# Optimization experiments

Measured on AMD Instinct MI355X. Metric: run time of the kernel, lower is better.

## Reference

```python
import jax, jax.numpy as jnp
import numpy as np

N_NODES = 100000
N_EDGES = 1600000
IN_FEATS = 128
OUT_FEATS = 128


def setup_inputs() -> dict:
    key = jax.random.key(0)
    k1, k2, k3, k4 = jax.random.split(key, 4)
    edge_data = jax.random.normal(k1, (N_EDGES, IN_FEATS), dtype=jnp.float32)
    dst = jax.random.randint(k2, (N_EDGES,), 0, N_NODES, dtype=jnp.int32)
    # nn.Linear(in_feats, out_feats) init scale ~ 1/sqrt(in_feats)
    s = 1.0 / np.sqrt(IN_FEATS)
    W = jax.random.uniform(k3, (OUT_FEATS, IN_FEATS), dtype=jnp.float32, minval=-s, maxval=s)
    b = jax.random.uniform(k4, (OUT_FEATS,), dtype=jnp.float32, minval=-s, maxval=s)
    return {"edge_data": edge_data, "dst": dst, "W": W, "b": b}


def reference(edge_data, dst, W, b):
    # Segment-mean of edge features into destination-node mailboxes.
    # DGL: h[v] = mean over incoming edges' 'h'; then ReLU(W h + b).
    sums = jax.ops.segment_sum(edge_data, dst, num_segments=N_NODES)  # [N, in]
    counts = jax.ops.segment_sum(jnp.ones((N_EDGES,), jnp.float32), dst,
                                 num_segments=N_NODES)  # [N]
    agg = sums / jnp.maximum(counts, 1.0)[:, None]  # mean; 0 for isolated nodes
    h = agg @ W.T + b  # [N, out]
    return jax.nn.relu(h)
```

## Files before the change

### kernel.cpp

```cpp
#include <hip/hip_runtime.h>

#define NEDGES 1600000
#define NNODES 100000
#define NF 128
#define NBUCK 391
#define NBLKA 391
#define NOFF  (NBUCK * NBLKA)
#define NSB   150

typedef short s16x8 __attribute__((ext_vector_type(8)));
typedef float f32x4 __attribute__((ext_vector_type(4)));

#define BH_B     0u
#define BHO_B    611584u
#define SST_B    1223168u
#define ROWPTR_B 1224448u
#define BKT_B    1624512u
#define EIDS_B   8024512u
#define WBF_B    14424512u

static __device__ __forceinline__ unsigned short f2bf(float x) {
    unsigned u = __float_as_uint(x);
    return (unsigned short)((u + 0x7fffu + ((u >> 16) & 1u)) >> 16);
}

__global__ __launch_bounds__(256) void k_bhist(const int* __restrict__ dst,
                                               int* __restrict__ bh,
                                               const float* __restrict__ W,
                                               unsigned short* __restrict__ Wb) {
    __shared__ int cnt[NBUCK];
    const int t = threadIdx.x, b = blockIdx.x;
    const int g = b * 256 + t;
    if (g < NF * NF) Wb[g] = f2bf(W[g]);
    for (int k = t; k < NBUCK; k += 256) cnt[k] = 0;
    __syncthreads();
    const int base = b * 4096;
    #pragma unroll
    for (int j = 0; j < 4; ++j) {
        const int i = base + j * 1024 + t * 4;
        if (i + 4 <= NEDGES) {
            const int4 d = *(const int4*)(dst + i);
            atomicAdd(&cnt[d.x >> 8], 1);
            atomicAdd(&cnt[d.y >> 8], 1);
            atomicAdd(&cnt[d.z >> 8], 1);
            atomicAdd(&cnt[d.w >> 8], 1);
        } else {
            for (int e = i; e < NEDGES; ++e) atomicAdd(&cnt[dst[e] >> 8], 1);
        }
    }
    __syncthreads();
    for (int k = t; k < NBUCK; k += 256) bh[k * NBLKA + b] = cnt[k];
}

__global__ __launch_bounds__(256) void k_scanB(const int* __restrict__ in,
                                               int* __restrict__ outp,
                                               unsigned long long* __restrict__ state) {
    const int t = threadIdx.x, b = blockIdx.x;
    const int lane = t & 63, wv = t >> 6;
    const int i0 = b * 1024 + t * 4;
    int v0 = 0, v1 = 0, v2 = 0, v3 = 0;
    if (i0 + 4 <= NOFF) {
        const int4 q = *(const int4*)(in + i0);
        v0 = q.x; v1 = q.y; v2 = q.z; v3 = q.w;
    } else if (i0 < NOFF) {
        v0 = in[i0];
        if (i0 + 1 < NOFF) v1 = in[i0 + 1];
        if (i0 + 2 < NOFF) v2 = in[i0 + 2];
    }
    const int tsum = v0 + v1 + v2 + v3;
    int winc = tsum;
    #pragma unroll
    for (int d = 1; d < 64; d <<= 1) {
        const int u = __shfl_up(winc, d, 64);
        if (lane >= d) winc += u;
    }
    __shared__ int wsum[4];
    __shared__ int xbase;
    if (lane == 63) wsum[wv] = winc;
    __syncthreads();
    int woff = 0;
    #pragma unroll
    for (int w = 0; w < 3; ++w)
        if (wv > w) woff += wsum[w];
    const int tot = wsum[0] + wsum[1] + wsum[2] + wsum[3];

    if (wv == 0) {
        if (b > 0) {
            if (lane == 0)
                __hip_atomic_store(&state[b],
                                   ((unsigned long long)1 << 32) | (unsigned)tot,
                                   __ATOMIC_RELEASE, __HIP_MEMORY_SCOPE_AGENT);
            int excl = 0;
            int p = b - 1;
            for (;;) {
                const int idx = p - lane;
                unsigned long long s;
                do {
                    s = (idx >= 0)
                        ? __hip_atomic_load(&state[idx], __ATOMIC_ACQUIRE,
                                            __HIP_MEMORY_SCOPE_AGENT)
                        : ((unsigned long long)2 << 32);
                    if (!(s >> 32)) __builtin_amdgcn_s_sleep(2);
                } while (__any(!(s >> 32)));
                const unsigned long long m2 = __ballot((s >> 32) == 2);
                const int f = m2 ? (__ffsll((long long)m2) - 1) : 63;
                int c = (lane <= f) ? (int)(unsigned)s : 0;
                #pragma unroll
                for (int d = 32; d > 0; d >>= 1) c += __shfl_xor(c, d, 64);
                excl += c;
                if (m2) break;
                p -= 64;
            }
            if (lane == 0) {
                __hip_atomic_store(&state[b],
                                   ((unsigned long long)2 << 32) |
                                       (unsigned)(excl + tot),
                                   __ATOMIC_RELEASE, __HIP_MEMORY_SCOPE_AGENT);
                xbase = excl;
            }
        } else {
            if (lane == 0) {
                __hip_atomic_store(&state[0],
                                   ((unsigned long long)2 << 32) | (unsigned)tot,
                                   __ATOMIC_RELEASE, __HIP_MEMORY_SCOPE_AGENT);
                xbase = 0;
            }
        }
    }
    __syncthreads();

    const int base = xbase + woff + (winc - tsum);
    if (i0 + 4 <= NOFF) {
        int4 r;
        r.x = base; r.y = base + v0; r.z = base + v0 + v1; r.w = base + v0 + v1 + v2;
        *(int4*)(outp + i0) = r;
    } else if (i0 < NOFF) {
        outp[i0] = base;
        if (i0 + 1 < NOFF) outp[i0 + 1] = base + v0;
        if (i0 + 2 < NOFF) outp[i0 + 2] = base + v0 + v1;
    }
}

__global__ __launch_bounds__(256) void k_scatterA(const int* __restrict__ dst,
                                                  const int* __restrict__ bhoff,
                                                  unsigned* __restrict__ bucketed) {
    __shared__ int cur[NBUCK];
    const int t = threadIdx.x, b = blockIdx.x;
    for (int k = t; k < NBUCK; k += 256) cur[k] = 0;
    __syncthreads();
    const int base = b * 4096;
    #pragma unroll
    for (int j = 0; j < 4; ++j) {
        const int i = base + j * 1024 + t * 4;
        if (i + 4 <= NEDGES) {
            const int4 d = *(const int4*)(dst + i);
            const int r0 = atomicAdd(&cur[d.x >> 8], 1);
            const int r1 = atomicAdd(&cur[d.y >> 8], 1);
            const int r2 = atomicAdd(&cur[d.z >> 8], 1);
            const int r3 = atomicAdd(&cur[d.w >> 8], 1);
            bucketed[bhoff[(d.x >> 8) * NBLKA + b] + r0] =
                ((unsigned)(i + 0) << 8) | (unsigned)(d.x & 255);
            bucketed[bhoff[(d.y >> 8) * NBLKA + b] + r1] =
                ((unsigned)(i + 1) << 8) | (unsigned)(d.y & 255);
            bucketed[bhoff[(d.z >> 8) * NBLKA + b] + r2] =
                ((unsigned)(i + 2) << 8) | (unsigned)(d.z & 255);
            bucketed[bhoff[(d.w >> 8) * NBLKA + b] + r3] =
                ((unsigned)(i + 3) << 8) | (unsigned)(d.w & 255);
        } else {
            for (int e = i; e < NEDGES; ++e) {
                const int d = dst[e];
                const int r = atomicAdd(&cur[d >> 8], 1);
                bucketed[bhoff[(d >> 8) * NBLKA + b] + r] =
                    ((unsigned)e << 8) | (unsigned)(d & 255);
            }
        }
    }
}

__global__ __launch_bounds__(256) void k_bucket(const unsigned* __restrict__ bucketed,
                                                const int* __restrict__ bhoff,
                                                int* __restrict__ rowptr,
                                                unsigned* __restrict__ eids) {
    __shared__ int cnt[256], rnk[256], exc[256];
    __shared__ int wtot[4];
    const int t = threadIdx.x, k = blockIdx.x;
    const int lane = t & 63, wv = t >> 6;
    cnt[t] = 0;
    rnk[t] = 0;
    __syncthreads();
    const int ebase = bhoff[k * NBLKA];
    const int eend  = (k + 1 < NBUCK) ? bhoff[(k + 1) * NBLKA] : NEDGES;
    const int ecnt  = eend - ebase;

    for (int i = t; i < ecnt; i += 256)
        atomicAdd(&cnt[bucketed[ebase + i] & 255u], 1);
    __syncthreads();

    const int own = cnt[t];
    int incl = own;
    #pragma unroll
    for (int d = 1; d < 64; d <<= 1) {
        const int u = __shfl_up(incl, d, 64);
        if (lane >= d) incl += u;
    }
    if (lane == 63) wtot[wv] = incl;
    __syncthreads();
    int woff = 0;
    #pragma unroll
    for (int w = 0; w < 3; ++w)
        if (wv > w) woff += wtot[w];
    exc[t] = woff + incl - own;
    __syncthreads();

    const int node = k * 256 + t;
    if (node < NNODES) rowptr[node] = ebase + exc[t];
    if (k == 0 && t == 0) rowptr[NNODES] = NEDGES;

    for (int i = t; i < ecnt; i += 256) {
        const unsigned u = bucketed[ebase + i];
        const int local = (int)(u & 255u);
        const int r = atomicAdd(&rnk[local], 1);
        eids[ebase + exc[local] + r] = ((u >> 8) << 4) | (unsigned)(local & 15);
    }
}

__global__ __launch_bounds__(256) void k_fused(
        const float* __restrict__ edge, const int* __restrict__ rowptr,
        const unsigned* __restrict__ eids, const unsigned short* __restrict__ Wb,
        const float* __restrict__ bias, float* __restrict__ out) {
    __shared__ float aggf[16][132];
    __shared__ __align__(16) char aggb[16 * 256];
    const int tid  = threadIdx.x;
    const int lane = tid & 63;
    const int wv   = tid >> 6;
    const int l15  = lane & 15;
    const int l4   = lane >> 4;
    const int n0   = blockIdx.x * 16;

    for (int idx = tid; idx < 16 * 132; idx += 256)
        (&aggf[0][0])[idx] = 0.0f;
    __syncthreads();

    const int eb    = rowptr[n0];
    const int ee    = rowptr[n0 + 16];
    const int chunk = (ee - eb + 3) >> 2;
    const int wcs   = eb + wv * chunk;
    const int wce   = min(wcs + chunk, ee);

    int   cur = -1;
    float a0 = 0.f, a1 = 0.f;

    for (int base = wcs; base < wce; base += 64) {
        const int m = min(64, wce - base);
        const unsigned ev = (lane < m) ? eids[base + lane] : 0u;
        int b = 0;
        for (; b + 16 <= m; b += 16) {
            unsigned id[16];
            int      rw[16];
            #pragma unroll
            for (int j = 0; j < 16; ++j) {
                const unsigned u = (unsigned)__builtin_amdgcn_readlane((int)ev, b + j);
                id[j] = u >> 4;
                rw[j] = (int)(u & 15u);
            }
            float2 xv[16];
            #pragma unroll
            for (int j = 0; j < 16; ++j)
                xv[j] = *(const float2*)(edge + (size_t)id[j] * NF + lane * 2);
            #pragma unroll
            for (int j = 0; j < 16; ++j) {
                if (rw[j] != cur) {
                    if (cur >= 0) {
                        atomicAdd(&aggf[cur][lane], a0);
                        atomicAdd(&aggf[cur][64 + lane], a1);
                    }
                    cur = rw[j];
                    a0 = 0.f; a1 = 0.f;
                }
                a0 += xv[j].x;
                a1 += xv[j].y;
            }
        }
        for (; b < m; ++b) {
            const unsigned u = (unsigned)__builtin_amdgcn_readlane((int)ev, b);
            const float2 v = *(const float2*)(edge + (size_t)(u >> 4) * NF + lane * 2);
            const int r = (int)(u & 15u);
            if (r != cur) {
                if (cur >= 0) {
                    atomicAdd(&aggf[cur][lane], a0);
                    atomicAdd(&aggf[cur][64 + lane], a1);
                }
                cur = r;
                a0 = 0.f; a1 = 0.f;
            }
            a0 += v.x;
            a1 += v.y;
        }
    }
    if (cur >= 0) {
        atomicAdd(&aggf[cur][lane], a0);
        atomicAdd(&aggf[cur][64 + lane], a1);
    }
    __syncthreads();

    {
        const int r  = tid >> 4;
        const int p0 = (tid & 15) * 4;
        const int cs = rowptr[n0 + r];
        const int ce = rowptr[n0 + r + 1];
        const float inv = 1.0f / fmaxf((float)(ce - cs), 1.0f);
        const float4 xv = *(const float4*)&aggf[r][p0];
        const float4 yv = *(const float4*)&aggf[r][64 + p0];
        const float xa[4] = {xv.x, xv.y, xv.z, xv.w};
        const float ya[4] = {yv.x, yv.y, yv.z, yv.w};
        #pragma unroll
        for (int j = 0; j < 4; ++j) {
            const unsigned pk = (unsigned)f2bf(xa[j] * inv) |
                                ((unsigned)f2bf(ya[j] * inv) << 16);
            const int byt = ((r * 256 + (p0 + j) * 4) ^ ((r & 7) << 4));
            *(unsigned*)(aggb + byt) = pk;
        }
    }
    __syncthreads();

    #pragma unroll
    for (int t = 0; t < 2; ++t) {
        const int j0 = (wv * 2 + t) * 16;
        f32x4 acc = {0.f, 0.f, 0.f, 0.f};
        #pragma unroll
        for (int ks = 0; ks < 4; ++ks) {
            const s16x8 wfv = *(const s16x8*)((const char*)Wb +
                                              (j0 + l15) * 256 + ks * 64 + l4 * 16);
            const int byt = ((l15 * 256 + ks * 64 + l4 * 16) ^ ((l15 & 7) << 4));
            const s16x8 av = *(const s16x8*)(aggb + byt);
            acc = __builtin_amdgcn_mfma_f32_16x16x32_bf16(av, wfv, acc, 0, 0, 0);
        }
        const float bj = bias[j0 + l15];
        #pragma unroll
        for (int r = 0; r < 4; ++r) {
            const int m = l4 * 4 + r;
            out[(size_t)(n0 + m) * NF + j0 + l15] = fmaxf(acc[r] + bj, 0.f);
        }
    }
}

extern "C" void kernel_launch(void* const* d_in, const int* in_sizes, int n_in,
                              void* d_out, int out_size, void* d_ws, size_t ws_size,
                              hipStream_t stream) {
    const float* edge = (const float*)d_in[0];
    const int*   dst  = (const int*)d_in[1];
    const float* W    = (const float*)d_in[2];
    const float* b    = (const float*)d_in[3];
    float* out = (float*)d_out;

    char* ws = (char*)d_ws;
    int*                bh       = (int*)(ws + BH_B);
    int*                bhoff    = (int*)(ws + BHO_B);
    unsigned long long* sstate   = (unsigned long long*)(ws + SST_B);
    int*                rowptr   = (int*)(ws + ROWPTR_B);
    unsigned*           bucketed = (unsigned*)(ws + BKT_B);
    unsigned*           eids     = (unsigned*)(ws + EIDS_B);
    unsigned short*     Wb       = (unsigned short*)(ws + WBF_B);

    hipMemsetAsync(ws + SST_B, 0, 1280, stream);

    k_bhist<<<NBLKA, 256, 0, stream>>>(dst, bh, W, Wb);
    k_scanB<<<NSB, 256, 0, stream>>>(bh, bhoff, sstate);
    k_scatterA<<<NBLKA, 256, 0, stream>>>(dst, bhoff, bucketed);
    k_bucket<<<NBUCK, 256, 0, stream>>>(bucketed, bhoff, rowptr, eids);
    k_fused<<<NNODES / 16, 256, 0, stream>>>(edge, rowptr, eids, Wb, b, out);
}
```

Before: 240.2 us.

## Fold scan-state memset into histogram kernel, use nontemporal accesses, coalesce output stores

```diff
diff --git a/kernel.cpp b/kernel.cpp
--- a/kernel.cpp
+++ b/kernel.cpp
@@ -27,11 +27,13 @@
 __global__ __launch_bounds__(256) void k_bhist(const int* __restrict__ dst,
                                                int* __restrict__ bh,
                                                const float* __restrict__ W,
-                                               unsigned short* __restrict__ Wb) {
+                                               unsigned short* __restrict__ Wb,
+                                               unsigned long long* __restrict__ sstate) {
     __shared__ int cnt[NBUCK];
     const int t = threadIdx.x, b = blockIdx.x;
     const int g = b * 256 + t;
     if (g < NF * NF) Wb[g] = f2bf(W[g]);
+    if (b == 0 && t < 160) sstate[t] = 0ull;
     for (int k = t; k < NBUCK; k += 256) cnt[k] = 0;
     __syncthreads();
     const int base = b * 4096;
@@ -158,14 +160,14 @@
             const int r1 = atomicAdd(&cur[d.y >> 8], 1);
             const int r2 = atomicAdd(&cur[d.z >> 8], 1);
             const int r3 = atomicAdd(&cur[d.w >> 8], 1);
-            bucketed[bhoff[(d.x >> 8) * NBLKA + b] + r0] =
-                ((unsigned)(i + 0) << 8) | (unsigned)(d.x & 255);
-            bucketed[bhoff[(d.y >> 8) * NBLKA + b] + r1] =
-                ((unsigned)(i + 1) << 8) | (unsigned)(d.y & 255);
-            bucketed[bhoff[(d.z >> 8) * NBLKA + b] + r2] =
-                ((unsigned)(i + 2) << 8) | (unsigned)(d.z & 255);
-            bucketed[bhoff[(d.w >> 8) * NBLKA + b] + r3] =
-                ((unsigned)(i + 3) << 8) | (unsigned)(d.w & 255);
+            __builtin_nontemporal_store(((unsigned)(i + 0) << 8) | (unsigned)(d.x & 255),
+                                        bucketed + bhoff[(d.x >> 8) * NBLKA + b] + r0);
+            __builtin_nontemporal_store(((unsigned)(i + 1) << 8) | (unsigned)(d.y & 255),
+                                        bucketed + bhoff[(d.y >> 8) * NBLKA + b] + r1);
+            __builtin_nontemporal_store(((unsigned)(i + 2) << 8) | (unsigned)(d.z & 255),
+                                        bucketed + bhoff[(d.z >> 8) * NBLKA + b] + r2);
+            __builtin_nontemporal_store(((unsigned)(i + 3) << 8) | (unsigned)(d.w & 255),
+                                        bucketed + bhoff[(d.w >> 8) * NBLKA + b] + r3);
         } else {
             for (int e = i; e < NEDGES; ++e) {
                 const int d = dst[e];
@@ -220,7 +222,8 @@
         const unsigned u = bucketed[ebase + i];
         const int local = (int)(u & 255u);
         const int r = atomicAdd(&rnk[local], 1);
-        eids[ebase + exc[local] + r] = ((u >> 8) << 4) | (unsigned)(local & 15);
+        __builtin_nontemporal_store(((u >> 8) << 4) | (unsigned)(local & 15),
+                                    eids + ebase + exc[local] + r);
     }
 }
 
@@ -265,8 +268,11 @@
             }
             float2 xv[16];
             #pragma unroll
-            for (int j = 0; j < 16; ++j)
-                xv[j] = *(const float2*)(edge + (size_t)id[j] * NF + lane * 2);
+            for (int j = 0; j < 16; ++j) {
+                const double dv = __builtin_nontemporal_load(
+                    (const double*)(edge + (size_t)id[j] * NF + lane * 2));
+                __builtin_memcpy(&xv[j], &dv, 8);
+            }
             #pragma unroll
             for (int j = 0; j < 16; ++j) {
                 if (rw[j] != cur) {
@@ -339,8 +345,19 @@
         #pragma unroll
         for (int r = 0; r < 4; ++r) {
             const int m = l4 * 4 + r;
-            out[(size_t)(n0 + m) * NF + j0 + l15] = fmaxf(acc[r] + bj, 0.f);
-        }
+            aggf[m][j0 + l15] = fmaxf(acc[r] + bj, 0.f);
+        }
+    }
+    __syncthreads();
+
+    {
+        const int r  = tid >> 4;
+        const int c0 = (tid & 15) * 8;
+        float4 v0 = *(const float4*)&aggf[r][c0];
+        float4 v1 = *(const float4*)&aggf[r][c0 + 4];
+        float* dst = out + (size_t)(n0 + r) * NF + c0;
+        *(float4*)dst       = v0;
+        *(float4*)(dst + 4) = v1;
     }
 }
 
@@ -362,9 +379,7 @@
     unsigned*           eids     = (unsigned*)(ws + EIDS_B);
     unsigned short*     Wb       = (unsigned short*)(ws + WBF_B);
 
-    hipMemsetAsync(ws + SST_B, 0, 1280, stream);
-
-    k_bhist<<<NBLKA, 256, 0, stream>>>(dst, bh, W, Wb);
+    k_bhist<<<NBLKA, 256, 0, stream>>>(dst, bh, W, Wb, sstate);
     k_scanB<<<NSB, 256, 0, stream>>>(bh, bhoff, sstate);
     k_scatterA<<<NBLKA, 256, 0, stream>>>(dst, bhoff, bucketed);
     k_bucket<<<NBUCK, 256, 0, stream>>>(bucketed, bhoff, rowptr, eids);
```

After: 312.5 us. +30.1%, slower.
